# Kernel tuning notes

Measured on AMD Instinct MI355X. Metric: run time of the kernel, lower is better.

Reference implementation:

```python
import jax, jax.numpy as jnp
import numpy as np

N = 50000          # nodes
E = 640000         # edges (before self-loops)
DIM_FEATS = 128
DIM_H = 32
HEADS1 = 8
NUM_CLASS = 16
NEG_SLOPE_ATT = 0.2   # PyG GATv2Conv default negative_slope
NEG_SLOPE_OUT = 0.01  # F.leaky_relu default


def setup_inputs() -> dict:
    key = jax.random.key(0)
    ks = jax.random.split(key, 12)
    s = 0.1
    x = jax.random.normal(ks[0], (N, DIM_FEATS), dtype=jnp.float32)
    edge_index = jax.random.randint(ks[1], (2, E), 0, N, dtype=jnp.int32)
    # GATv2Conv layer 1: dim_feats -> dim_h per head, 8 heads, concat
    W1l = jax.random.normal(ks[2], (DIM_FEATS, HEADS1 * DIM_H), dtype=jnp.float32) * s
    W1r = jax.random.normal(ks[3], (DIM_FEATS, HEADS1 * DIM_H), dtype=jnp.float32) * s
    att1 = jax.random.normal(ks[4], (HEADS1, DIM_H), dtype=jnp.float32) * s
    b1 = jnp.zeros((HEADS1 * DIM_H,), dtype=jnp.float32)
    # GATv2Conv layer 2: 256 -> num_class, 1 head, concat=False
    W2l = jax.random.normal(ks[5], (HEADS1 * DIM_H, NUM_CLASS), dtype=jnp.float32) * s
    W2r = jax.random.normal(ks[6], (HEADS1 * DIM_H, NUM_CLASS), dtype=jnp.float32) * s
    att2 = jax.random.normal(ks[7], (1, NUM_CLASS), dtype=jnp.float32) * s
    b2 = jnp.zeros((NUM_CLASS,), dtype=jnp.float32)
    return {"x": x, "edge_index": edge_index, "W1l": W1l, "W1r": W1r,
            "att1": att1, "b1": b1, "W2l": W2l, "W2r": W2r,
            "att2": att2, "b2": b2}


def _segment_softmax(scores, seg, num_segments):
    # scores: [E, H], seg: [E] destination node ids
    m = jax.ops.segment_max(scores, seg, num_segments=num_segments)  # [N, H]
    e = jnp.exp(scores - m[seg])
    denom = jax.ops.segment_sum(e, seg, num_segments=num_segments)   # [N, H]
    return e / (denom[seg] + 1e-16)


def _gatv2_layer(x, src, dst, Wl, Wr, att, bias, heads, out_ch, concat):
    n = x.shape[0]
    xl = (x @ Wl).reshape(n, heads, out_ch)  # source transform
    xr = (x @ Wr).reshape(n, heads, out_ch)  # target transform
    # per-edge GATv2 score: a^T LeakyReLU(xl[j] + xr[i])
    e = jax.nn.leaky_relu(xl[src] + xr[dst], negative_slope=NEG_SLOPE_ATT)  # [E,H,F]
    alpha = jnp.einsum('ehf,hf->eh', e, att)                                # [E,H]
    alpha = _segment_softmax(alpha, dst, n)
    msg = xl[src] * alpha[:, :, None]                                       # [E,H,F]
    out = jax.ops.segment_sum(msg, dst, num_segments=n)                     # [N,H,F]
    out = out.reshape(n, heads * out_ch) if concat else out.mean(axis=1)
    return out + bias


def reference(x, edge_index, W1l, W1r, att1, b1, W2l, W2r, att2, b2):
    # add_self_loops=True (PyG GATv2Conv default)
    loop = jnp.arange(N, dtype=edge_index.dtype)
    src = jnp.concatenate([edge_index[0], loop])
    dst = jnp.concatenate([edge_index[1], loop])
    # eval mode: all dropouts are identity
    h = _gatv2_layer(x, src, dst, W1l, W1r, att1, b1, HEADS1, DIM_H, concat=True)
    h = jax.nn.elu(h)
    h = _gatv2_layer(h, src, dst, W2l, W2r, att2, b2, 1, NUM_CLASS, concat=False)
    return jax.nn.leaky_relu(h, negative_slope=NEG_SLOPE_OUT)
```

## Files before the change

kernel.cpp:

```cpp
#include <hip/hip_runtime.h>
#include <math.h>

#define NN 50000
#define E0 640000
#define ET 690000
#define F1 128
#define D1 256
#define C2 16
#define NB 196
#define MPAD 50048
#define PADK 136
#define LOG2E 1.4426950408889634f
#define NBK1 782
#define GEMMB 782

typedef _Float16 f16x8 __attribute__((ext_vector_type(8)));
typedef _Float16 h2 __attribute__((ext_vector_type(2)));
typedef __attribute__((ext_vector_type(4))) float f32x4;

__device__ __forceinline__ unsigned short f2h(float f) {
  union { _Float16 h; unsigned short u; } c;
  c.h = (_Float16)f;
  return c.u;
}
__device__ __forceinline__ float h2f(unsigned short u) {
  union { unsigned short u; _Float16 h; } c; c.u = u; return (float)c.h;
}
__device__ __forceinline__ h2 u2h2(unsigned u) {
  union { unsigned u; h2 h; } c; c.u = u; return c.h;
}
__device__ __forceinline__ unsigned h22u(h2 h) {
  union { h2 h; unsigned u; } c; c.h = h; return c.u;
}

template <int CTRL>
__device__ __forceinline__ float dpp_add(float c) {
  int t = __builtin_amdgcn_update_dpp(0, __builtin_bit_cast(int, c), CTRL, 0xF, 0xF, true);
  return c + __builtin_bit_cast(float, t);
}
template <int K>
__device__ __forceinline__ int dpp_bcast(int v) {
  constexpr int ctrl = K | (K << 2) | (K << 4) | (K << 6);
  return __builtin_amdgcn_update_dpp(0, v, ctrl, 0xF, 0xF, true);
}

__global__ __launch_bounds__(256) void k_prep(
    const float* __restrict__ Wl, const float* __restrict__ Wr,
    const float* __restrict__ W2l, const float* __restrict__ W2r,
    const int* __restrict__ ei,
    unsigned short* __restrict__ wt, unsigned short* __restrict__ wt2,
    int* __restrict__ deg) {
  const int b = blockIdx.x;
  if (b < 256) {
    int tid = b * 256 + threadIdx.x;
    int n = tid >> 7, k = tid & 127;
    float v = (n < 256) ? Wl[k * 256 + n] : Wr[k * 256 + (n - 256)];
    wt[tid] = f2h(v);
  } else if (b < 288) {
    int tid = (b - 256) * 256 + threadIdx.x;
    int n = tid >> 8, k = tid & 255;
    float v = (n < 16) ? W2l[k * 16 + n] : W2r[k * 16 + (n - 16)];
    wt2[tid] = f2h(v);
  } else {
    int e = (b - 288) * 256 + threadIdx.x;
    if (e >= ET) return;
    int d = (e < E0) ? ei[E0 + e] : (e - E0);
    atomicAdd(&deg[d], 1);
  }
}

__global__ __launch_bounds__(256) void k_scan_part(const int* __restrict__ deg,
                                                   int* __restrict__ part) {
  int i = blockIdx.x * 256 + threadIdx.x;
  int v = (i < NN) ? deg[i] : 0;
  v += __shfl_xor(v, 1);  v += __shfl_xor(v, 2);  v += __shfl_xor(v, 4);
  v += __shfl_xor(v, 8);  v += __shfl_xor(v, 16); v += __shfl_xor(v, 32);
  __shared__ int w[4];
  if ((threadIdx.x & 63) == 0) w[threadIdx.x >> 6] = v;
  __syncthreads();
  if (threadIdx.x == 0) part[blockIdx.x] = w[0] + w[1] + w[2] + w[3];
}

__global__ __launch_bounds__(256) void k_scan_apply(int* __restrict__ deg,
                                                    const int* __restrict__ part,
                                                    int* __restrict__ offs,
                                                    uint2* __restrict__ ninfo,
                                                    unsigned short* __restrict__ csr) {
  __shared__ int lds[256];
  __shared__ int red[4];
  const int b = blockIdx.x, t = threadIdx.x;
  const int i = b * 256 + t;
  int v = (i < NN) ? deg[i] : 0;
  lds[t] = v;
  int pp = 0;
  for (int j = t; j < b; j += 256) pp += part[j];
  pp += __shfl_xor(pp, 1);  pp += __shfl_xor(pp, 2);  pp += __shfl_xor(pp, 4);
  pp += __shfl_xor(pp, 8);  pp += __shfl_xor(pp, 16); pp += __shfl_xor(pp, 32);
  if ((t & 63) == 0) red[t >> 6] = pp;
  __syncthreads();
  const int prefix = red[0] + red[1] + red[2] + red[3];
  for (int off = 1; off < 256; off <<= 1) {
    int u = (t >= off) ? lds[t - off] : 0;
    __syncthreads();
    lds[t] += u;
    __syncthreads();
  }
  int excl = prefix + lds[t] - v;
  if (i < NN) {
    offs[i] = excl;
    deg[i] = excl + 1;
    csr[excl] = (unsigned short)i;
    ninfo[i] = make_uint2((unsigned)excl, (unsigned)i | ((unsigned)v << 16));
  }
  if (b == NB - 1 && t == 255) offs[NN] = prefix + lds[255];
}

__global__ __launch_bounds__(256) void k_gemm1s(
    const float* __restrict__ x, const unsigned short* __restrict__ wt,
    unsigned short* __restrict__ xlh, unsigned short* __restrict__ xrh,
    const int* __restrict__ ei, int* __restrict__ cur,
    unsigned short* __restrict__ csr) {
  __shared__ unsigned short Al[64 * PADK];
  __shared__ unsigned short Bl[128 * PADK];
  if (blockIdx.x >= GEMMB) {
    int e = (blockIdx.x - GEMMB) * 256 + threadIdx.x;
    if (e < E0) {
      int s = ei[e], d = ei[E0 + e];
      int pos = atomicAdd(&cur[d], 1);
      csr[pos] = (unsigned short)s;
    }
    return;
  }
  const int t = threadIdx.x;
  const int m0 = blockIdx.x * 64;
  {
    const int r = t >> 4;
    const int c = (t & 15) * 8;
#pragma unroll
    for (int p = 0; p < 4; ++p) {
      const int row = r + p * 16;
      const int rg = m0 + row;
      const float* xp = &x[(size_t)(rg < NN ? rg : NN - 1) * F1 + c];
      float4 lo = *(const float4*)xp;
      float4 hi = *(const float4*)(xp + 4);
      h2 q0 = h2{(_Float16)lo.x, (_Float16)lo.y};
      h2 q1 = h2{(_Float16)lo.z, (_Float16)lo.w};
      h2 q2 = h2{(_Float16)hi.x, (_Float16)hi.y};
      h2 q3 = h2{(_Float16)hi.z, (_Float16)hi.w};
      uint4 st; st.x = h22u(q0); st.y = h22u(q1); st.z = h22u(q2); st.w = h22u(q3);
      *(uint4*)&Al[row * PADK + c] = st;
    }
  }
  const int wave = t >> 6, lane = t & 63;
  const int mw = (wave >> 1) * 32, nw = (wave & 1) * 64;
  const int fr = lane & 15, fq = lane >> 4;
  for (int ny = 0; ny < 4; ++ny) {
    const int n0 = ny * 128;
    {
      const int r = t >> 4;
      const int c = (t & 15) * 8;
#pragma unroll
      for (int p = 0; p < 8; ++p) {
        const int row = r + p * 16;
        *(float4*)&Bl[row * PADK + c] = *(const float4*)&wt[(size_t)(n0 + row) * F1 + c];
      }
    }
    __syncthreads();
    f32x4 acc[2][4] = {};
#pragma unroll
    for (int ks = 0; ks < 4; ++ks) {
      const int ko = ks * 32 + fq * 8;
      f16x8 a[2], b[4];
#pragma unroll
      for (int i = 0; i < 2; ++i)
        a[i] = *(const f16x8*)&Al[(mw + i * 16 + fr) * PADK + ko];
#pragma unroll
      for (int j = 0; j < 4; ++j)
        b[j] = *(const f16x8*)&Bl[(nw + j * 16 + fr) * PADK + ko];
#pragma unroll
      for (int i = 0; i < 2; ++i)
#pragma unroll
        for (int j = 0; j < 4; ++j)
          acc[i][j] = __builtin_amdgcn_mfma_f32_16x16x32_f16(a[i], b[j], acc[i][j], 0, 0, 0);
    }
    __syncthreads();
    unsigned short* outp = (n0 < 256) ? xlh : xrh;
    const int cb = (n0 & 255) + nw + fr;
#pragma unroll
    for (int j = 0; j < 4; ++j) {
      const int col = cb + j * 16;
      const int head = col >> 5, f = col & 31;
      unsigned short* hp = outp + (size_t)head * NN * 32 + f;
#pragma unroll
      for (int i = 0; i < 2; ++i) {
        const int gm0 = m0 + mw + i * 16 + fq * 4;
#pragma unroll
        for (int r = 0; r < 4; ++r) {
          const int gm = gm0 + r;
          if (gm < NN) hp[(size_t)gm * 32] = f2h(acc[i][j][r]);
        }
      }
    }
  }
}

__global__ __launch_bounds__(256) void k_agg1(
    const unsigned short* __restrict__ xlh, const unsigned short* __restrict__ xrh,
    unsigned short* __restrict__ hb,
    const uint2* __restrict__ ninfo, const unsigned short* __restrict__ csr,
    const float* __restrict__ att, const float* __restrict__ b1) {
  const int b = blockIdx.x;
  const int head = b & 7;
  const int wave = threadIdx.x >> 6;
  const int lane = threadIdx.x & 63;
  const int g = lane >> 2;
  const int j4 = lane & 3;
  const int idxn = (b >> 3) * 64 + wave * 16 + g;
  const bool valid = idxn < NN;
  const int n = valid ? idxn : 0;
  const int colh = j4 * 8;
  const int col = head * 32 + colh;
  const unsigned short* xlhead = xlh + (size_t)head * NN * 32;

  const uint2 nf = ninfo[n];
  const int beg = (int)nf.x;
  const int fin = valid ? beg + (int)(nf.y >> 16) : beg;

  const uint4 xru = *(const uint4*)&xrh[((size_t)head * NN + n) * 32 + colh];
  h2 xr2[4];
  xr2[0] = u2h2(xru.x); xr2[1] = u2h2(xru.y);
  xr2[2] = u2h2(xru.z); xr2[3] = u2h2(xru.w);
  float at8[8];
  *(float4*)&at8[0] = *(const float4*)&att[col];
  *(float4*)&at8[4] = *(const float4*)&att[col + 4];
  h2 ath6[4], ath4[4];
#pragma unroll
  for (int j = 0; j < 4; ++j) {
    ath6[j] = h2{(_Float16)(at8[2 * j] * (0.6f * LOG2E)),
                 (_Float16)(at8[2 * j + 1] * (0.6f * LOG2E))};
    ath4[j] = h2{(_Float16)(at8[2 * j] * (0.4f * LOG2E)),
                 (_Float16)(at8[2 * j + 1] * (0.4f * LOG2E))};
  }
  float l = 0.f;
  h2 acc2[4] = {h2{0, 0}, h2{0, 0}, h2{0, 0}, h2{0, 0}};

  auto ldids = [&](int base) -> int {
    int a = base + j4;
    a = (a < fin) ? a : beg;
    return (int)csr[a];
  };
  auto XLrow = [&](int s) -> uint4 {
    return *(const uint4*)&xlhead[(size_t)s * 32 + colh];
  };
  auto edge = [&](const uint4& w, bool live) {
    h2 xh[4];
    xh[0] = u2h2(w.x); xh[1] = u2h2(w.y); xh[2] = u2h2(w.z); xh[3] = u2h2(w.w);
    float cv = 0.f, ca = 0.f;
#pragma unroll
    for (int j = 0; j < 4; ++j) {
      h2 v = xh[j] + xr2[j];
      h2 a = u2h2(h22u(v) & 0x7FFF7FFFu);
      cv = __builtin_amdgcn_fdot2(v, ath6[j], cv, false);
      ca = __builtin_amdgcn_fdot2(a, ath4[j], ca, false);
    }
    float c = cv + ca;
    c = dpp_add<0xB1>(c);
    c = dpp_add<0x4E>(c);
    float p = exp2f(c);
    p = live ? p : 0.f;
    l += p;
    const _Float16 ph = (_Float16)p;
    const h2 p2 = h2{ph, ph};
#pragma unroll
    for (int j = 0; j < 4; ++j) acc2[j] += p2 * xh[j];
  };

  int ids = ldids(beg);
  uint4 w0 = XLrow(dpp_bcast<0>(ids));
  uint4 w1 = XLrow(dpp_bcast<1>(ids));
  uint4 w2 = XLrow(dpp_bcast<2>(ids));
  uint4 w3 = XLrow(dpp_bcast<3>(ids));
  int ids1 = ldids(beg + 4);
  for (int idx = beg; idx < fin; idx += 4) {
    const uint4 v0 = XLrow(dpp_bcast<0>(ids1));
    const uint4 v1 = XLrow(dpp_bcast<1>(ids1));
    const uint4 v2 = XLrow(dpp_bcast<2>(ids1));
    const uint4 v3 = XLrow(dpp_bcast<3>(ids1));
    const int ids2 = ldids(idx + 8);
    edge(w0, true);
    edge(w1, idx + 1 < fin);
    edge(w2, idx + 2 < fin);
    edge(w3, idx + 3 < fin);
    w0 = v0; w1 = v1; w2 = v2; w3 = v3; ids1 = ids2;
  }

  if (valid) {
    const float rl = __builtin_amdgcn_rcpf(l + 1e-16f);
    float b8[8], o[8];
    *(float4*)&b8[0] = *(const float4*)&b1[col];
    *(float4*)&b8[4] = *(const float4*)&b1[col + 4];
#pragma unroll
    for (int j = 0; j < 4; ++j) {
      o[2 * j]     = (float)acc2[j][0] * rl + b8[2 * j];
      o[2 * j + 1] = (float)acc2[j][1] * rl + b8[2 * j + 1];
    }
#pragma unroll
    for (int k = 0; k < 8; ++k)
      o[k] = o[k] > 0.f ? o[k] : exp2f(o[k] * LOG2E) - 1.f;
    ushort4 p;
    p.x = f2h(o[0]); p.y = f2h(o[1]); p.z = f2h(o[2]); p.w = f2h(o[3]);
    ushort4 q;
    q.x = f2h(o[4]); q.y = f2h(o[5]); q.z = f2h(o[6]); q.w = f2h(o[7]);
    uint4 packed;
    packed.x = *(unsigned*)&p.x; packed.y = *(unsigned*)&p.z;
    packed.z = *(unsigned*)&q.x; packed.w = *(unsigned*)&q.z;
    *(uint4*)&hb[(size_t)n * D1 + col] = packed;
  }
}

__global__ __launch_bounds__(256) void k_gemm2m(
    const unsigned short* __restrict__ hb, const unsigned short* __restrict__ wt2,
    unsigned short* __restrict__ h2lh, float* __restrict__ h2r) {
  const int t = threadIdx.x;
  const int wave = t >> 6, lane = t & 63;
  const int fr = lane & 15, fq = lane >> 4;
  const int m0 = blockIdx.x * 128 + wave * 32;
  f32x4 acc[2][2] = {};
#pragma unroll
  for (int ks = 0; ks < 8; ++ks) {
    const int ko = ks * 32 + fq * 8;
    f16x8 a[2], b[2];
#pragma unroll
    for (int i = 0; i < 2; ++i) {
      int row = m0 + i * 16 + fr; if (row >= NN) row = NN - 1;
      a[i] = *(const f16x8*)&hb[(size_t)row * D1 + ko];
    }
#pragma unroll
    for (int j = 0; j < 2; ++j)
      b[j] = *(const f16x8*)&wt2[(j * 16 + fr) * 256 + ko];
#pragma unroll
    for (int i = 0; i < 2; ++i)
#pragma unroll
      for (int j = 0; j < 2; ++j)
        acc[i][j] = __builtin_amdgcn_mfma_f32_16x16x32_f16(a[i], b[j], acc[i][j], 0, 0, 0);
  }
#pragma unroll
  for (int i = 0; i < 2; ++i) {
    const int gm0 = m0 + i * 16 + fq * 4;
#pragma unroll
    for (int r = 0; r < 4; ++r) {
      const int gm = gm0 + r;
      if (gm < NN) {
        h2lh[(size_t)gm * C2 + fr] = f2h(acc[i][0][r]);
        h2r[(size_t)gm * C2 + fr] = acc[i][1][r];
      }
    }
  }
}

__global__ __launch_bounds__(256) void k_agg2(
    const unsigned short* __restrict__ h2lh, const float* __restrict__ h2r,
    const int* __restrict__ offs, const unsigned short* __restrict__ csr,
    const float* __restrict__ att2, const float* __restrict__ b2,
    float* __restrict__ out) {
  const int wave = threadIdx.x >> 6;
  const int lane = threadIdx.x & 63;
  const int n = blockIdx.x * 4 + wave;
  if (n >= NN) return;
  const int c = lane & 15, g = lane >> 4;
  const float xr_v = h2r[(size_t)n * C2 + c];
  const float att_v = att2[c] * LOG2E;
  float l = 0.f, acc = 0.f;
  const int beg = offs[n], fin = offs[n + 1];
  for (int idx = beg + g; idx < fin; idx += 8) {
    const int i1 = idx + 4;
    const bool m1 = i1 < fin;
    const int s0 = csr[idx];
    const int s1 = csr[m1 ? i1 : idx];
    const float xl0 = h2f(h2lh[(size_t)s0 * C2 + c]);
    const float xl1 = h2f(h2lh[(size_t)s1 * C2 + c]);
    float v0 = xl0 + xr_v; v0 = fmaxf(v0, 0.2f * v0);
    float v1 = xl1 + xr_v; v1 = fmaxf(v1, 0.2f * v1);
    float sc0 = v0 * att_v, sc1 = v1 * att_v;
    sc0 = dpp_add<0xB1>(sc0);   sc1 = dpp_add<0xB1>(sc1);
    sc0 = dpp_add<0x4E>(sc0);   sc1 = dpp_add<0x4E>(sc1);
    sc0 = dpp_add<0x124>(sc0);  sc1 = dpp_add<0x124>(sc1);
    sc0 = dpp_add<0x128>(sc0);  sc1 = dpp_add<0x128>(sc1);
    const float p0 = exp2f(sc0);
    const float p1 = m1 ? exp2f(sc1) : 0.f;
    l += p0 + p1;
    acc = fmaf(p0, xl0, fmaf(p1, xl1, acc));
  }
  l += __shfl_xor(l, 16);   l += __shfl_xor(l, 32);
  acc += __shfl_xor(acc, 16); acc += __shfl_xor(acc, 32);
  float o = acc * __builtin_amdgcn_rcpf(l + 1e-16f) + b2[c];
  o = o > 0.f ? o : 0.01f * o;
  if (lane < 16) out[(size_t)n * C2 + c] = o;
}

extern "C" void kernel_launch(void* const* d_in, const int* in_sizes, int n_in,
                              void* d_out, int out_size, void* d_ws, size_t ws_size,
                              hipStream_t stream) {
  const float* x    = (const float*)d_in[0];
  const int*   ei   = (const int*)d_in[1];
  const float* W1l  = (const float*)d_in[2];
  const float* W1r  = (const float*)d_in[3];
  const float* att1 = (const float*)d_in[4];
  const float* b1   = (const float*)d_in[5];
  const float* W2l  = (const float*)d_in[6];
  const float* W2r  = (const float*)d_in[7];
  const float* att2 = (const float*)d_in[8];
  const float* b2   = (const float*)d_in[9];
  float* out = (float*)d_out;

  unsigned short* xlh = (unsigned short*)d_ws;
  unsigned short* xrh = xlh + (size_t)NN * D1;
  unsigned short* hb  = xrh + (size_t)NN * D1;
  int* deg  = (int*)(hb + (size_t)NN * D1);
  int* part = deg + NN;
  int* offs = part + NB;
  uint2* ninfo = (uint2*)(offs + NN + 2);
  unsigned short* csr = (unsigned short*)(ninfo + NN);
  unsigned short* wt  = csr + ET + 2;
  unsigned short* wt2 = wt + 512 * F1;
  unsigned short* h2lh = xlh;
  float* h2r = (float*)(h2lh + (size_t)NN * C2);

  hipMemsetAsync(deg, 0, NN * sizeof(int), stream);
  k_prep<<<288 + (ET + 255) / 256, 256, 0, stream>>>(
      W1l, W1r, W2l, W2r, ei, wt, wt2, deg);
  k_scan_part<<<NB, 256, 0, stream>>>(deg, part);
  k_scan_apply<<<NB, 256, 0, stream>>>(deg, part, offs, ninfo, csr);
  k_gemm1s<<<GEMMB + (E0 + 255) / 256, 256, 0, stream>>>(
      x, wt, xlh, xrh, ei, deg, csr);
  k_agg1<<<NBK1 * 8, 256, 0, stream>>>(xlh, xrh, hb, ninfo, csr, att1, b1);
  k_gemm2m<<<(NN + 127) / 128, 256, 0, stream>>>(hb, wt2, h2lh, h2r);
  k_agg2<<<NN / 4, 256, 0, stream>>>(h2lh, h2r, offs, csr, att2, b2, out);
}
```

Measured before the change: 261.8 us.

## Split layer-1 GEMM from CSR scatter and stage output through LDS for vector stores

The fused GEMM+scatter kernel is split into a standalone GEMM kernel, launched before the scan, and a separate scatter kernel. The new GEMM reads weight fragments directly from global memory instead of staging B in LDS. It transposes results through an LDS tile so each thread writes 16-byte contiguous rows per head instead of scattered 2-byte stores. The cost is an extra launch and extra LDS round-trips, and B fragments may now see uncoalesced global loads.

```diff
diff --git a/kernel.cpp b/kernel.cpp
--- a/kernel.cpp
+++ b/kernel.cpp
@@ -10,9 +10,9 @@
 #define NB 196
 #define MPAD 50048
 #define PADK 136
+#define TPAD 40
 #define LOG2E 1.4426950408889634f
 #define NBK1 782
-#define GEMMB 782
 
 typedef _Float16 f16x8 __attribute__((ext_vector_type(8)));
 typedef _Float16 h2 __attribute__((ext_vector_type(2)));
@@ -66,6 +66,84 @@
     if (e >= ET) return;
     int d = (e < E0) ? ei[E0 + e] : (e - E0);
     atomicAdd(&deg[d], 1);
+  }
+}
+
+__global__ __launch_bounds__(256) void k_gemm1m(
+    const float* __restrict__ x, const unsigned short* __restrict__ wt,
+    unsigned short* __restrict__ xlh, unsigned short* __restrict__ xrh) {
+  __shared__ unsigned short Al[64 * PADK];
+  __shared__ unsigned short T[256 * TPAD];
+  const int t = threadIdx.x;
+  const int m0 = blockIdx.x * 64;
+  {
+    const int r = t >> 4;
+    const int c = (t & 15) * 8;
+#pragma unroll
+    for (int p = 0; p < 4; ++p) {
+      const int row = r + p * 16;
+      const int rg = m0 + row;
+      const float* xp = &x[(size_t)(rg < NN ? rg : NN - 1) * F1 + c];
+      float4 lo = *(const float4*)xp;
+      float4 hi = *(const float4*)(xp + 4);
+      h2 q0 = h2{(_Float16)lo.x, (_Float16)lo.y};
+      h2 q1 = h2{(_Float16)lo.z, (_Float16)lo.w};
+      h2 q2 = h2{(_Float16)hi.x, (_Float16)hi.y};
+      h2 q3 = h2{(_Float16)hi.z, (_Float16)hi.w};
+      uint4 st; st.x = h22u(q0); st.y = h22u(q1); st.z = h22u(q2); st.w = h22u(q3);
+      *(uint4*)&Al[row * PADK + c] = st;
+    }
+  }
+  __syncthreads();
+  const int wave = t >> 6, lane = t & 63;
+  const int mw = (wave >> 1) * 32, nw = (wave & 1) * 64;
+  const int fr = lane & 15, fq = lane >> 4;
+  const int mS = t >> 2, qS = t & 3;
+  for (int ny = 0; ny < 4; ++ny) {
+    const int n0 = ny * 128;
+    f32x4 acc[2][4] = {};
+#pragma unroll
+    for (int ks = 0; ks < 4; ++ks) {
+      const int ko = ks * 32 + fq * 8;
+      f16x8 a[2], b[4];
+#pragma unroll
+      for (int i = 0; i < 2; ++i)
+        a[i] = *(const f16x8*)&Al[(mw + i * 16 + fr) * PADK + ko];
+#pragma unroll
+      for (int j = 0; j < 4; ++j)
+        b[j] = *(const f16x8*)&wt[(size_t)(n0 + nw + j * 16 + fr) * F1 + ko];
+#pragma unroll
+      for (int i = 0; i < 2; ++i)
+#pragma unroll
+        for (int j = 0; j < 4; ++j)
+          acc[i][j] = __builtin_amdgcn_mfma_f32_16x16x32_f16(a[i], b[j], acc[i][j], 0, 0, 0);
+    }
+    __syncthreads();
+#pragma unroll
+    for (int j = 0; j < 4; ++j) {
+      const int cpan = nw + j * 16 + fr;
+      const int hl = cpan >> 5, f = cpan & 31;
+#pragma unroll
+      for (int i = 0; i < 2; ++i) {
+        const int mrow = mw + i * 16 + fq * 4;
+#pragma unroll
+        for (int r = 0; r < 4; ++r)
+          T[(hl * 64 + mrow + r) * TPAD + f] = f2h(acc[i][j][r]);
+      }
+    }
+    __syncthreads();
+    unsigned short* outp = (n0 < 256) ? xlh : xrh;
+    const int head0 = (ny & 1) * 4;
+    const int gm = m0 + mS;
+    if (gm < NN) {
+      const unsigned short* src = &T[mS * TPAD + qS * 8];
+#pragma unroll
+      for (int hl = 0; hl < 4; ++hl) {
+        unsigned short* dst =
+            outp + (size_t)(head0 + hl) * NN * 32 + (size_t)gm * 32 + qS * 8;
+        *(uint4*)dst = *(const uint4*)(src + hl * 64 * TPAD);
+      }
+    }
   }
 }
 
@@ -115,93 +193,13 @@
   if (b == NB - 1 && t == 255) offs[NN] = prefix + lds[255];
 }
 
-__global__ __launch_bounds__(256) void k_gemm1s(
-    const float* __restrict__ x, const unsigned short* __restrict__ wt,
-    unsigned short* __restrict__ xlh, unsigned short* __restrict__ xrh,
-    const int* __restrict__ ei, int* __restrict__ cur,
-    unsigned short* __restrict__ csr) {
-  __shared__ unsigned short Al[64 * PADK];
-  __shared__ unsigned short Bl[128 * PADK];
-  if (blockIdx.x >= GEMMB) {
-    int e = (blockIdx.x - GEMMB) * 256 + threadIdx.x;
-    if (e < E0) {
-      int s = ei[e], d = ei[E0 + e];
-      int pos = atomicAdd(&cur[d], 1);
-      csr[pos] = (unsigned short)s;
-    }
-    return;
-  }
-  const int t = threadIdx.x;
-  const int m0 = blockIdx.x * 64;
-  {
-    const int r = t >> 4;
-    const int c = (t & 15) * 8;
-#pragma unroll
-    for (int p = 0; p < 4; ++p) {
-      const int row = r + p * 16;
-      const int rg = m0 + row;
-      const float* xp = &x[(size_t)(rg < NN ? rg : NN - 1) * F1 + c];
-      float4 lo = *(const float4*)xp;
-      float4 hi = *(const float4*)(xp + 4);
-      h2 q0 = h2{(_Float16)lo.x, (_Float16)lo.y};
-      h2 q1 = h2{(_Float16)lo.z, (_Float16)lo.w};
-      h2 q2 = h2{(_Float16)hi.x, (_Float16)hi.y};
-      h2 q3 = h2{(_Float16)hi.z, (_Float16)hi.w};
-      uint4 st; st.x = h22u(q0); st.y = h22u(q1); st.z = h22u(q2); st.w = h22u(q3);
-      *(uint4*)&Al[row * PADK + c] = st;
-    }
-  }
-  const int wave = t >> 6, lane = t & 63;
-  const int mw = (wave >> 1) * 32, nw = (wave & 1) * 64;
-  const int fr = lane & 15, fq = lane >> 4;
-  for (int ny = 0; ny < 4; ++ny) {
-    const int n0 = ny * 128;
-    {
-      const int r = t >> 4;
-      const int c = (t & 15) * 8;
-#pragma unroll
-      for (int p = 0; p < 8; ++p) {
-        const int row = r + p * 16;
-        *(float4*)&Bl[row * PADK + c] = *(const float4*)&wt[(size_t)(n0 + row) * F1 + c];
-      }
-    }
-    __syncthreads();
-    f32x4 acc[2][4] = {};
-#pragma unroll
-    for (int ks = 0; ks < 4; ++ks) {
-      const int ko = ks * 32 + fq * 8;
-      f16x8 a[2], b[4];
-#pragma unroll
-      for (int i = 0; i < 2; ++i)
-        a[i] = *(const f16x8*)&Al[(mw + i * 16 + fr) * PADK + ko];
-#pragma unroll
-      for (int j = 0; j < 4; ++j)
-        b[j] = *(const f16x8*)&Bl[(nw + j * 16 + fr) * PADK + ko];
-#pragma unroll
-      for (int i = 0; i < 2; ++i)
-#pragma unroll
-        for (int j = 0; j < 4; ++j)
-          acc[i][j] = __builtin_amdgcn_mfma_f32_16x16x32_f16(a[i], b[j], acc[i][j], 0, 0, 0);
-    }
-    __syncthreads();
-    unsigned short* outp = (n0 < 256) ? xlh : xrh;
-    const int cb = (n0 & 255) + nw + fr;
-#pragma unroll
-    for (int j = 0; j < 4; ++j) {
-      const int col = cb + j * 16;
-      const int head = col >> 5, f = col & 31;
-      unsigned short* hp = outp + (size_t)head * NN * 32 + f;
-#pragma unroll
-      for (int i = 0; i < 2; ++i) {
-        const int gm0 = m0 + mw + i * 16 + fq * 4;
-#pragma unroll
-        for (int r = 0; r < 4; ++r) {
-          const int gm = gm0 + r;
-          if (gm < NN) hp[(size_t)gm * 32] = f2h(acc[i][j][r]);
-        }
-      }
-    }
-  }
+__global__ void k_scatter(const int* __restrict__ ei, int* __restrict__ cur,
+                          unsigned short* __restrict__ csr) {
+  int e = blockIdx.x * 256 + threadIdx.x;
+  if (e >= E0) return;
+  int s = ei[e], d = ei[E0 + e];
+  int pos = atomicAdd(&cur[d], 1);
+  csr[pos] = (unsigned short)s;
 }
 
 __global__ __launch_bounds__(256) void k_agg1(
@@ -429,10 +427,10 @@
   hipMemsetAsync(deg, 0, NN * sizeof(int), stream);
   k_prep<<<288 + (ET + 255) / 256, 256, 0, stream>>>(
       W1l, W1r, W2l, W2r, ei, wt, wt2, deg);
+  k_gemm1m<<<MPAD / 64, 256, 0, stream>>>(x, wt, xlh, xrh);
   k_scan_part<<<NB, 256, 0, stream>>>(deg, part);
   k_scan_apply<<<NB, 256, 0, stream>>>(deg, part, offs, ninfo, csr);
-  k_gemm1s<<<GEMMB + (E0 + 255) / 256, 256, 0, stream>>>(
-      x, wt, xlh, xrh, ei, deg, csr);
+  k_scatter<<<(E0 + 255) / 256, 256, 0, stream>>>(ei, deg, csr);
   k_agg1<<<NBK1 * 8, 256, 0, stream>>>(xlh, xrh, hb, ninfo, csr, att1, b1);
   k_gemm2m<<<(NN + 127) / 128, 256, 0, stream>>>(hb, wt2, h2lh, h2r);
   k_agg2<<<NN / 4, 256, 0, stream>>>(h2lh, h2r, offs, csr, att2, b2, out);
```

Result: slower. 272.5 us (+4.1%).

## Sort nodes by degree within blocks for agg1 balance and split edge scatter

Applied to the files above, without the earlier changes.

The scan kernel now buckets the nodes of each 256-node block by descending degree and writes ninfo in that order. k_agg1 then reads the node id from ninfo, so lanes handling neighbouring groups get similar edge counts and wavefront divergence drops. The edge-scatter work, previously fused into the layer-1 GEMM launch, moves to its own kernel, and the GEMM is moved ahead of the scan. The cost is one extra kernel launch and some LDS atomics during the scan.

```diff
diff --git a/kernel.cpp b/kernel.cpp
--- a/kernel.cpp
+++ b/kernel.cpp
@@ -12,7 +12,6 @@
 #define PADK 136
 #define LOG2E 1.4426950408889634f
 #define NBK1 782
-#define GEMMB 782
 
 typedef _Float16 f16x8 __attribute__((ext_vector_type(8)));
 typedef _Float16 h2 __attribute__((ext_vector_type(2)));
@@ -69,68 +68,11 @@
   }
 }
 
-__global__ __launch_bounds__(256) void k_scan_part(const int* __restrict__ deg,
-                                                   int* __restrict__ part) {
-  int i = blockIdx.x * 256 + threadIdx.x;
-  int v = (i < NN) ? deg[i] : 0;
-  v += __shfl_xor(v, 1);  v += __shfl_xor(v, 2);  v += __shfl_xor(v, 4);
-  v += __shfl_xor(v, 8);  v += __shfl_xor(v, 16); v += __shfl_xor(v, 32);
-  __shared__ int w[4];
-  if ((threadIdx.x & 63) == 0) w[threadIdx.x >> 6] = v;
-  __syncthreads();
-  if (threadIdx.x == 0) part[blockIdx.x] = w[0] + w[1] + w[2] + w[3];
-}
-
-__global__ __launch_bounds__(256) void k_scan_apply(int* __restrict__ deg,
-                                                    const int* __restrict__ part,
-                                                    int* __restrict__ offs,
-                                                    uint2* __restrict__ ninfo,
-                                                    unsigned short* __restrict__ csr) {
-  __shared__ int lds[256];
-  __shared__ int red[4];
-  const int b = blockIdx.x, t = threadIdx.x;
-  const int i = b * 256 + t;
-  int v = (i < NN) ? deg[i] : 0;
-  lds[t] = v;
-  int pp = 0;
-  for (int j = t; j < b; j += 256) pp += part[j];
-  pp += __shfl_xor(pp, 1);  pp += __shfl_xor(pp, 2);  pp += __shfl_xor(pp, 4);
-  pp += __shfl_xor(pp, 8);  pp += __shfl_xor(pp, 16); pp += __shfl_xor(pp, 32);
-  if ((t & 63) == 0) red[t >> 6] = pp;
-  __syncthreads();
-  const int prefix = red[0] + red[1] + red[2] + red[3];
-  for (int off = 1; off < 256; off <<= 1) {
-    int u = (t >= off) ? lds[t - off] : 0;
-    __syncthreads();
-    lds[t] += u;
-    __syncthreads();
-  }
-  int excl = prefix + lds[t] - v;
-  if (i < NN) {
-    offs[i] = excl;
-    deg[i] = excl + 1;
-    csr[excl] = (unsigned short)i;
-    ninfo[i] = make_uint2((unsigned)excl, (unsigned)i | ((unsigned)v << 16));
-  }
-  if (b == NB - 1 && t == 255) offs[NN] = prefix + lds[255];
-}
-
-__global__ __launch_bounds__(256) void k_gemm1s(
+__global__ __launch_bounds__(256) void k_gemm1m(
     const float* __restrict__ x, const unsigned short* __restrict__ wt,
-    unsigned short* __restrict__ xlh, unsigned short* __restrict__ xrh,
-    const int* __restrict__ ei, int* __restrict__ cur,
-    unsigned short* __restrict__ csr) {
+    unsigned short* __restrict__ xlh, unsigned short* __restrict__ xrh) {
   __shared__ unsigned short Al[64 * PADK];
   __shared__ unsigned short Bl[128 * PADK];
-  if (blockIdx.x >= GEMMB) {
-    int e = (blockIdx.x - GEMMB) * 256 + threadIdx.x;
-    if (e < E0) {
-      int s = ei[e], d = ei[E0 + e];
-      int pos = atomicAdd(&cur[d], 1);
-      csr[pos] = (unsigned short)s;
-    }
-    return;
-  }
   const int t = threadIdx.x;
   const int m0 = blockIdx.x * 64;
   {
@@ -202,6 +144,81 @@
       }
     }
   }
+}
+
+__global__ __launch_bounds__(256) void k_scan_part(const int* __restrict__ deg,
+                                                   int* __restrict__ part) {
+  int i = blockIdx.x * 256 + threadIdx.x;
+  int v = (i < NN) ? deg[i] : 0;
+  v += __shfl_xor(v, 1);  v += __shfl_xor(v, 2);  v += __shfl_xor(v, 4);
+  v += __shfl_xor(v, 8);  v += __shfl_xor(v, 16); v += __shfl_xor(v, 32);
+  __shared__ int w[4];
+  if ((threadIdx.x & 63) == 0) w[threadIdx.x >> 6] = v;
+  __syncthreads();
+  if (threadIdx.x == 0) part[blockIdx.x] = w[0] + w[1] + w[2] + w[3];
+}
+
+__global__ __launch_bounds__(256) void k_scan_apply(int* __restrict__ deg,
+                                                    const int* __restrict__ part,
+                                                    int* __restrict__ offs,
+                                                    uint2* __restrict__ ninfo,
+                                                    unsigned short* __restrict__ csr) {
+  __shared__ int lds[256];
+  __shared__ int red[4];
+  __shared__ int bh[64];
+  __shared__ int bb[64];
+  const int b = blockIdx.x, t = threadIdx.x;
+  const int i = b * 256 + t;
+  int v = (i < NN) ? deg[i] : 0;
+  lds[t] = v;
+  if (t < 64) bh[t] = 0;
+  int pp = 0;
+  for (int j = t; j < b; j += 256) pp += part[j];
+  pp += __shfl_xor(pp, 1);  pp += __shfl_xor(pp, 2);  pp += __shfl_xor(pp, 4);
+  pp += __shfl_xor(pp, 8);  pp += __shfl_xor(pp, 16); pp += __shfl_xor(pp, 32);
+  if ((t & 63) == 0) red[t >> 6] = pp;
+  __syncthreads();
+  int bkt = 0, lpos = 0;
+  if (i < NN) {
+    bkt = 63 - (v < 63 ? v : 63);
+    lpos = atomicAdd(&bh[bkt], 1);
+  }
+  const int prefix = red[0] + red[1] + red[2] + red[3];
+  for (int off = 1; off < 256; off <<= 1) {
+    int u = (t >= off) ? lds[t - off] : 0;
+    __syncthreads();
+    lds[t] += u;
+    __syncthreads();
+  }
+  int excl = prefix + lds[t] - v;
+  if (i < NN) {
+    offs[i] = excl;
+    deg[i] = excl + 1;
+    csr[excl] = (unsigned short)i;
+  }
+  if (b == NB - 1 && t == 255) offs[NN] = prefix + lds[255];
+  if (t < 64) {
+    int xv = bh[t];
+    int s = xv;
+    for (int off = 1; off < 64; off <<= 1) {
+      int u = __shfl_up(s, off);
+      if (t >= off) s += u;
+    }
+    bb[t] = s - xv;
+  }
+  __syncthreads();
+  if (i < NN)
+    ninfo[b * 256 + bb[bkt] + lpos] =
+        make_uint2((unsigned)excl, (unsigned)i | ((unsigned)v << 16));
+}
+
+__global__ void k_scatter(const int* __restrict__ ei, int* __restrict__ cur,
+                          unsigned short* __restrict__ csr) {
+  int e = blockIdx.x * 256 + threadIdx.x;
+  if (e >= E0) return;
+  int s = ei[e], d = ei[E0 + e];
+  int pos = atomicAdd(&cur[d], 1);
+  csr[pos] = (unsigned short)s;
 }
 
 __global__ __launch_bounds__(256) void k_agg1(
@@ -217,12 +234,12 @@
   const int j4 = lane & 3;
   const int idxn = (b >> 3) * 64 + wave * 16 + g;
   const bool valid = idxn < NN;
-  const int n = valid ? idxn : 0;
   const int colh = j4 * 8;
   const int col = head * 32 + colh;
   const unsigned short* xlhead = xlh + (size_t)head * NN * 32;
 
-  const uint2 nf = ninfo[n];
+  const uint2 nf = ninfo[valid ? idxn : 0];
+  const int n = (int)(nf.y & 0xFFFFu);
   const int beg = (int)nf.x;
   const int fin = valid ? beg + (int)(nf.y >> 16) : beg;
 
@@ -429,10 +446,10 @@
   hipMemsetAsync(deg, 0, NN * sizeof(int), stream);
   k_prep<<<288 + (ET + 255) / 256, 256, 0, stream>>>(
       W1l, W1r, W2l, W2r, ei, wt, wt2, deg);
+  k_gemm1m<<<MPAD / 64, 256, 0, stream>>>(x, wt, xlh, xrh);
   k_scan_part<<<NB, 256, 0, stream>>>(deg, part);
   k_scan_apply<<<NB, 256, 0, stream>>>(deg, part, offs, ninfo, csr);
-  k_gemm1s<<<GEMMB + (E0 + 255) / 256, 256, 0, stream>>>(
-      x, wt, xlh, xrh, ei, deg, csr);
+  k_scatter<<<(E0 + 255) / 256, 256, 0, stream>>>(ei, deg, csr);
   k_agg1<<<NBK1 * 8, 256, 0, stream>>>(xlh, xrh, hb, ninfo, csr, att1, b1);
   k_gemm2m<<<(NN + 127) / 128, 256, 0, stream>>>(hb, wt2, h2lh, h2r);
   k_agg2<<<NN / 4, 256, 0, stream>>>(h2lh, h2r, offs, csr, att2, b2, out);
```

Measured after the change: 262.8 us. No clear change (+0.4%).
